# Kernel optimization log

Measured on AMD Instinct MI355X. Metric: run time of the kernel, lower is better.

Reference implementation:

```python
import jax, jax.numpy as jnp
import numpy as np

B, T, U, D_DEC = 64, 4096, 256, 256

def setup_inputs() -> dict:
    key = jax.random.key(0)
    k1, k2, k3, k4 = jax.random.split(key, 4)
    encoder_h = jax.random.normal(k1, (B, T, U), dtype=jnp.float32)
    decoder_s = jax.random.normal(k2, (B, D_DEC), dtype=jnp.float32)
    # left-packed padding mask: valid tokens first (matches TF gather/pad-at-end semantics)
    lengths = jax.random.randint(k3, (B,), T // 4, T + 1)
    mask = (jnp.arange(T)[None, :] < lengths[:, None]).astype(jnp.int32)
    Wa_w = jax.random.normal(k4, (D_DEC, U), dtype=jnp.float32) / np.sqrt(D_DEC)
    Wa_b = jnp.zeros((U,), dtype=jnp.float32)
    return {"encoder_h": encoder_h, "decoder_s": decoder_s, "mask": mask,
            "Wa_w": Wa_w, "Wa_b": Wa_b}

def reference(encoder_h, decoder_s, mask, Wa_w, Wa_b):
    # state = Wa(decoder_s): [B, U]
    state = decoder_s @ Wa_w + Wa_b
    # score[b,t] = state[b] . encoder_h[b,t]  (Luong dot score)
    score = jnp.einsum('bu,btu->bt', state, encoder_h)
    m = mask > 0
    # masked softmax over valid (left-packed) positions; zeros on padding
    neg = jnp.finfo(score.dtype).min
    alpha = jax.nn.softmax(jnp.where(m, score, neg), axis=-1)
    alpha = jnp.where(m, alpha, jnp.zeros((), dtype=alpha.dtype))
    # context = sum_t alpha[b,t] * encoder_h[b,t]: [B, U]
    ct_sum = jnp.einsum('btu,bt->bu', encoder_h, alpha)
    return ct_sum, alpha[..., None]
```

## Files before the change

kernel.cpp:

```cpp
#include <hip/hip_runtime.h>

#define B 64
#define T 4096
#define U 256
#define SB 32
#define WPB 4
#define WBATCH (SB*WPB)

__global__ __launch_bounds__(256) void state_kernel(
    const float* __restrict__ ds, const float* __restrict__ W,
    const float* __restrict__ bias, float* __restrict__ state)
{
    const int b = blockIdx.x, u = threadIdx.x;
    __shared__ float ss[U];
    ss[u] = ds[b * U + u];
    __syncthreads();
    float acc = bias[u];
#pragma unroll 8
    for (int d = 0; d < U; ++d) acc = fmaf(ss[d], W[d * U + u], acc);
    state[b * U + u] = acc;
}

__global__ __launch_bounds__(256) void pass1(
    const float* __restrict__ h, const int* __restrict__ mask,
    const float* __restrict__ state, float* __restrict__ score,
    float* __restrict__ pm, float* __restrict__ pl, float* __restrict__ pacc)
{
    const int b    = blockIdx.x / SB;
    const int sblk = blockIdx.x % SB;
    const int tid  = threadIdx.x;
    const int wave = tid >> 6, lane = tid & 63;
    const int wi   = sblk * WPB + wave;

    const float4 st = *(const float4*)(state + b * U + (lane << 2));
    const float* hb = h + (size_t)b * T * U;
    const int*   mb = mask + b * T;
    float*      scb = score + (size_t)b * T;

    float  m = -INFINITY, l = 0.f;
    float4 acc = make_float4(0.f, 0.f, 0.f, 0.f);

    for (int t = wi; t < T; t += WBATCH) {
        if (mb[t] == 0) break;
        const float4 hv = *(const float4*)(hb + (size_t)t * U + (lane << 2));
        float p = st.x * hv.x + st.y * hv.y + st.z * hv.z + st.w * hv.w;
#pragma unroll
        for (int off = 32; off; off >>= 1) p += __shfl_xor(p, off, 64);
        if (lane == 0) scb[t] = p;
        const float nm = fmaxf(m, p);
        const float s0 = __expf(m - nm);
        const float e  = __expf(p - nm);
        l = l * s0 + e;
        acc.x = fmaf(acc.x, s0, e * hv.x);
        acc.y = fmaf(acc.y, s0, e * hv.y);
        acc.z = fmaf(acc.z, s0, e * hv.z);
        acc.w = fmaf(acc.w, s0, e * hv.w);
        m = nm;
    }

    __shared__ float sm[WPB], sl[WPB];
    __shared__ float sacc[WPB * U];
    *(float4*)&sacc[wave * U + (lane << 2)] = acc;
    if (lane == 0) { sm[wave] = m; sl[wave] = l; }
    __syncthreads();

    const float M = fmaxf(fmaxf(sm[0], sm[1]), fmaxf(sm[2], sm[3]));
    float Lb = 0.f, a = 0.f;
#pragma unroll
    for (int w = 0; w < WPB; ++w) {
        const float sc = __expf(sm[w] - M);
        Lb += sl[w] * sc;
        a  += sacc[w * U + tid] * sc;
    }
    const int pidx = b * SB + sblk;
    if (tid == 0) { pm[pidx] = M; pl[pidx] = Lb; }
    pacc[(size_t)pidx * U + tid] = a;
}

__global__ __launch_bounds__(256) void pass2(
    const int* __restrict__ mask, const float* __restrict__ pm,
    const float* __restrict__ pl, const float* __restrict__ pacc,
    float* __restrict__ ct, float* __restrict__ alpha)
{
    const int b = blockIdx.x, tid = threadIdx.x;
    float M = -INFINITY;
#pragma unroll
    for (int s = 0; s < SB; ++s) M = fmaxf(M, pm[b * SB + s]);
    float L = 0.f, a = 0.f;
#pragma unroll
    for (int s = 0; s < SB; ++s) {
        const float sc = __expf(pm[b * SB + s] - M);
        L += pl[b * SB + s] * sc;
        a += pacc[(size_t)(b * SB + s) * U + tid] * sc;
    }
    const float invL = 1.f / L;
    ct[b * U + tid] = a * invL;

    const int* mb = mask + b * T;
    float*     ab = alpha + (size_t)b * T;
    for (int t = tid; t < T; t += 256)
        ab[t] = mb[t] ? __expf(ab[t] - M) * invL : 0.f;
}

extern "C" void kernel_launch(void* const* d_in, const int* in_sizes, int n_in,
                              void* d_out, int out_size, void* d_ws, size_t ws_size,
                              hipStream_t stream) {
    const float* h    = (const float*)d_in[0];
    const float* ds   = (const float*)d_in[1];
    const int*   mask = (const int*)d_in[2];
    const float* W    = (const float*)d_in[3];
    const float* bias = (const float*)d_in[4];

    float* out   = (float*)d_out;
    float* ct    = out;
    float* alpha = out + B * U;

    float* ws    = (float*)d_ws;
    float* state = ws;
    float* pm    = state + B * U;
    float* pl    = pm + B * SB;
    float* pacc  = pl + B * SB;

    state_kernel<<<B, 256, 0, stream>>>(ds, W, bias, state);
    pass1<<<B * SB, 256, 0, stream>>>(h, mask, state, alpha, pm, pl, pacc);
    pass2<<<B, 256, 0, stream>>>(mask, pm, pl, pacc, ct, alpha);
}
```

Baseline: 373.4 us.

## Compute sequence length via ballot, prefetch next row, branchy online softmax, vectorize pass2

Pass1 now finds each batch's valid length up front with two wave ballots over the mask, replacing a per-iteration mask load and break. The loop software-prefetches the next encoder row while it processes the current one. The online softmax update branches so each step needs only one exp. Pass2 reads mask and alpha as int4/float4. The aim is to hide memory latency in the bandwidth-bound main loop, at the cost of extra registers and an assumption that the mask is left-packed.

```diff
diff --git a/kernel.cpp b/kernel.cpp
--- a/kernel.cpp
+++ b/kernel.cpp
@@ -32,30 +32,52 @@
     const int wave = tid >> 6, lane = tid & 63;
     const int wi   = sblk * WPB + wave;
 
+    const int* mb = mask + b * T;
+    const int s1 = mb[lane << 6];
+    const int k1 = __popcll(__ballot(s1 != 0));
+    const int base = (k1 - 1) << 6;
+    const int s2 = mb[base + lane];
+    const int len = base + __popcll(__ballot(s2 != 0));
+
     const float4 st = *(const float4*)(state + b * U + (lane << 2));
     const float* hb = h + (size_t)b * T * U;
-    const int*   mb = mask + b * T;
     float*      scb = score + (size_t)b * T;
 
     float  m = -INFINITY, l = 0.f;
     float4 acc = make_float4(0.f, 0.f, 0.f, 0.f);
 
-    for (int t = wi; t < T; t += WBATCH) {
-        if (mb[t] == 0) break;
-        const float4 hv = *(const float4*)(hb + (size_t)t * U + (lane << 2));
+    int t = wi;
+    float4 hv = make_float4(0.f, 0.f, 0.f, 0.f);
+    if (t < len) hv = *(const float4*)(hb + (size_t)t * U + (lane << 2));
+
+    while (t < len) {
+        const int tn = t + WBATCH;
+        const int tc = (tn < len) ? tn : t;
+        const float4 hn = *(const float4*)(hb + (size_t)tc * U + (lane << 2));
+
         float p = st.x * hv.x + st.y * hv.y + st.z * hv.z + st.w * hv.w;
 #pragma unroll
         for (int off = 32; off; off >>= 1) p += __shfl_xor(p, off, 64);
         if (lane == 0) scb[t] = p;
-        const float nm = fmaxf(m, p);
-        const float s0 = __expf(m - nm);
-        const float e  = __expf(p - nm);
-        l = l * s0 + e;
-        acc.x = fmaf(acc.x, s0, e * hv.x);
-        acc.y = fmaf(acc.y, s0, e * hv.y);
-        acc.z = fmaf(acc.z, s0, e * hv.z);
-        acc.w = fmaf(acc.w, s0, e * hv.w);
-        m = nm;
+
+        if (p > m) {
+            const float s0 = __expf(m - p);
+            l = fmaf(l, s0, 1.0f);
+            acc.x = fmaf(acc.x, s0, hv.x);
+            acc.y = fmaf(acc.y, s0, hv.y);
+            acc.z = fmaf(acc.z, s0, hv.z);
+            acc.w = fmaf(acc.w, s0, hv.w);
+            m = p;
+        } else {
+            const float e = __expf(p - m);
+            l += e;
+            acc.x = fmaf(e, hv.x, acc.x);
+            acc.y = fmaf(e, hv.y, acc.y);
+            acc.z = fmaf(e, hv.z, acc.z);
+            acc.w = fmaf(e, hv.w, acc.w);
+        }
+        hv = hn;
+        t  = tn;
     }
 
     __shared__ float sm[WPB], sl[WPB];
@@ -96,10 +118,17 @@
     const float invL = 1.f / L;
     ct[b * U + tid] = a * invL;
 
-    const int* mb = mask + b * T;
-    float*     ab = alpha + (size_t)b * T;
-    for (int t = tid; t < T; t += 256)
-        ab[t] = mb[t] ? __expf(ab[t] - M) * invL : 0.f;
+    const int4*   mb4 = (const int4*)(mask + b * T);
+    float4*       ab4 = (float4*)(alpha + (size_t)b * T);
+    for (int i = tid; i < T / 4; i += 256) {
+        const int4   mv = mb4[i];
+        float4       av = ab4[i];
+        av.x = mv.x ? __expf(av.x - M) * invL : 0.f;
+        av.y = mv.y ? __expf(av.y - M) * invL : 0.f;
+        av.z = mv.z ? __expf(av.z - M) * invL : 0.f;
+        av.w = mv.w ? __expf(av.w - M) * invL : 0.f;
+        ab4[i] = av;
+    }
 }
 
 extern "C" void kernel_launch(void* const* d_in, const int* in_sizes, int n_in,
```

Result: faster. 364.7 us (-2.3%).
